# Performance work log

Measured on AMD Instinct MI355X. Metric: run time of the kernel, lower is better.

Reference implementation:

```python
import jax, jax.numpy as jnp
import numpy as np

DIM = 256
HEADS = 8
HEAD_DIM = DIM // HEADS
SCALE = HEAD_DIM ** -0.5
B, H, W = 4, 48, 48


def setup_inputs() -> dict:
    key = jax.random.key(0)
    ks = jax.random.split(key, 10)
    s = 1.0 / np.sqrt(DIM)
    return {
        "img_features": jax.random.normal(ks[0], (B, DIM, H, W), jnp.float32),
        "radar_features": jax.random.normal(ks[1], (B, DIM, H, W), jnp.float32),
        "uncertainty_mask": jax.random.uniform(ks[2], (B, 1, H, W), jnp.float32),
        "Wq_img": jax.random.normal(ks[3], (DIM, DIM), jnp.float32) * s,
        "Wkv_radar": jax.random.normal(ks[4], (DIM, 2 * DIM), jnp.float32) * s,
        "Wq_radar": jax.random.normal(ks[5], (DIM, DIM), jnp.float32) * s,
        "Wkv_img": jax.random.normal(ks[6], (DIM, 2 * DIM), jnp.float32) * s,
        "Wp_img": jax.random.normal(ks[7], (DIM, DIM), jnp.float32) * s,
        "bp_img": jnp.zeros((DIM,), jnp.float32),
        "Wp_radar": jax.random.normal(ks[8], (DIM, DIM), jnp.float32) * s,
        "bp_radar": jnp.zeros((DIM,), jnp.float32),
    }


def _heads(x, b, n):
    # (B, N, C) -> (B, heads, N, head_dim)
    return x.reshape(b, n, HEADS, HEAD_DIM).transpose(0, 2, 1, 3)


def _cross_attn(q_seq, kv_seq, Wq, Wkv, uw=None):
    b, n, c = q_seq.shape
    q = _heads(q_seq @ Wq, b, n)                      # (B,h,N,d)
    kv = (kv_seq @ Wkv).reshape(b, n, 2, HEADS, HEAD_DIM)
    k = kv[:, :, 0].transpose(0, 2, 1, 3)             # (B,h,N,d)
    v = kv[:, :, 1].transpose(0, 2, 1, 3)
    scores = jnp.einsum("bhnd,bhmd->bhnm", q, k) * SCALE
    if uw is not None:
        scores = scores * uw                          # (B,1,N,1) broadcast
    p = jax.nn.softmax(scores, axis=-1)
    out = jnp.einsum("bhnm,bhmd->bhnd", p, v)
    return out.transpose(0, 2, 1, 3).reshape(b, n, c)


def reference(img_features, radar_features, uncertainty_mask,
              Wq_img, Wkv_radar, Wq_radar, Wkv_img,
              Wp_img, bp_img, Wp_radar, bp_radar):
    b, c, h, w = img_features.shape
    n = h * w
    img_seq = img_features.reshape(b, c, n).transpose(0, 2, 1)    # (B,N,C)
    radar_seq = radar_features.reshape(b, c, n).transpose(0, 2, 1)

    # uncertainty weight: (B,1,N,1), scales query rows before softmax
    u_seq = uncertainty_mask.reshape(b, 1, n).transpose(0, 2, 1)  # (B,N,1)
    uw = (1.0 / (u_seq + 1e-6))[:, None, :, :]

    img_att = _cross_attn(img_seq, radar_seq, Wq_img, Wkv_radar, uw)
    img_att = img_att @ Wp_img + bp_img

    radar_att = _cross_attn(radar_seq, img_seq, Wq_radar, Wkv_img, None)
    radar_att = radar_att @ Wp_radar + bp_radar

    img_out = img_att.transpose(0, 2, 1).reshape(b, c, h, w)
    radar_out = radar_att.transpose(0, 2, 1).reshape(b, c, h, w)
    return img_out, radar_out
```

## Files before the change

kernel.cpp:

```cpp
#include <hip/hip_runtime.h>
#include <math.h>

#define NB    4
#define CDIM  256
#define NSEQ  2304
#define NHEAD 8
#define HD    32
#define QSCALE (0.17677669529663687f * 1.4426950408889634f)
#define INV2048 4.8828125e-4f
#define FIXMAX 12.0f

typedef _Float16 f16;
typedef _Float16 f16x8 __attribute__((ext_vector_type(8)));
typedef _Float16 f16x4 __attribute__((ext_vector_type(4)));
typedef _Float16 f16x2 __attribute__((ext_vector_type(2)));
typedef float    f32x4 __attribute__((ext_vector_type(4)));
typedef float    f32x16 __attribute__((ext_vector_type(16)));
typedef unsigned u32x4 __attribute__((ext_vector_type(4)));

__device__ __forceinline__ float fast_exp2(float x) {
#if __has_builtin(__builtin_amdgcn_exp2f)
  return __builtin_amdgcn_exp2f(x);
#else
  return exp2f(x);
#endif
}

__device__ __forceinline__ unsigned pkrtz(float a, float b) {
#if __has_builtin(__builtin_amdgcn_cvt_pkrtz)
  auto h = __builtin_amdgcn_cvt_pkrtz(a, b);
  return __builtin_bit_cast(unsigned, h);
#else
  f16x2 h; h[0] = (f16)a; h[1] = (f16)b;
  return __builtin_bit_cast(unsigned, h);
#endif
}

__device__ __forceinline__ void plswap(unsigned &a, unsigned &b) {
#if __has_builtin(__builtin_amdgcn_permlane32_swap)
  auto r = __builtin_amdgcn_permlane32_swap(a, b, false, false);
  a = r[0]; b = r[1];
#else
  asm("v_permlane32_swap_b32 %0, %1" : "+v"(a), "+v"(b));
#endif
}

__device__ __forceinline__ float cross_fmax(float v) {
  unsigned a = __builtin_bit_cast(unsigned, v), b;
  asm("v_mov_b32 %0, %1" : "=v"(b) : "v"(a));
  plswap(a, b);
  return fmaxf(__builtin_bit_cast(float, a), __builtin_bit_cast(float, b));
}
__device__ __forceinline__ float cross_add(float v) {
  unsigned a = __builtin_bit_cast(unsigned, v), b;
  asm("v_mov_b32 %0, %1" : "=v"(b) : "v"(a));
  plswap(a, b);
  return __builtin_bit_cast(float, a) + __builtin_bit_cast(float, b);
}

__global__ __launch_bounds__(256) void prep_split(
    const float* __restrict__ X0, const float* __restrict__ X1,
    const float* __restrict__ Wq0, const float* __restrict__ Wkv0,
    const float* __restrict__ Wp0, const float* __restrict__ Wq1,
    const float* __restrict__ Wkv1, const float* __restrict__ Wp1,
    f16* __restrict__ X16h, f16* __restrict__ X16l,
    f16* __restrict__ WTh, f16* __restrict__ WTl)
{
  __shared__ float Ls[64][65];
  const int t = threadIdx.x;
  const int id = blockIdx.x;

  const float* in; int incols, c0, col0; size_t obase; f16 *oh, *ol;
  float scale = 1.f;
  if (id < 1152) {
    int mb = id / 144, rem = id % 144;
    int ct = rem / 36, nt = rem % 36;
    int mod = mb >> 2, b = mb & 3;
    in = (mod ? X1 : X0) + (size_t)b * 256 * NSEQ;
    incols = NSEQ; c0 = ct * 64; col0 = nt * 64;
    obase = (size_t)mb * NSEQ + col0;
    oh = X16h; ol = X16l;
  } else {
    int wid = id - 1152;
    int mod = wid >> 6, r = wid & 63;
    int jt, ct2, rowoff;
    if (r < 16) {
      in = mod ? Wq1 : Wq0; incols = 256; jt = r >> 2; ct2 = r & 3;
      rowoff = 0; scale = QSCALE;
    } else if (r < 48) {
      int rr = r - 16;
      in = mod ? Wkv1 : Wkv0; incols = 512; jt = rr >> 2; ct2 = rr & 3;
      rowoff = 256;
    } else {
      int rr = r - 48;
      in = mod ? Wp1 : Wp0; incols = 256; jt = rr >> 2; ct2 = rr & 3;
      rowoff = 768;
    }
    c0 = ct2 * 64; col0 = jt * 64;
    obase = (size_t)mod * 1024 + rowoff + col0;
    oh = WTh; ol = WTl;
  }

#pragma unroll
  for (int i = 0; i < 4; ++i) {
    int cl = (t >> 4) + i * 16;
    int n4 = (t & 15) * 4;
    *(float4*)&Ls[cl][n4] =
        *(const float4*)(in + (size_t)(c0 + cl) * incols + col0 + n4);
  }
  __syncthreads();
#pragma unroll
  for (int i = 0; i < 4; ++i) {
    int ll = (t >> 4) + i * 16;
    int c4 = (t & 15) * 4;
    f16x4 hv, lv;
#pragma unroll
    for (int j = 0; j < 4; ++j) {
      float v = Ls[c4 + j][ll] * scale;
      f16 hh = (f16)v;
      hv[j] = hh;
      lv[j] = (f16)((v - (float)hh) * 2048.0f);
    }
    size_t o = (obase + ll) * 256 + c0 + c4;
    *(f16x4*)(oh + o) = hv;
    *(f16x4*)(ol + o) = lv;
  }
}

__global__ __launch_bounds__(256) void proj_qkv_mfma(
    const f16* __restrict__ X16h, const f16* __restrict__ X16l,
    const f16* __restrict__ WTh, const f16* __restrict__ WTl,
    f16* __restrict__ Qh, f16* __restrict__ Ql,
    f16* __restrict__ Kh, f16* __restrict__ Kl, f16* __restrict__ Vt)
{
  __shared__ f16 WhS[128][32];
  __shared__ f16 WlS[128][32];
  __shared__ f16 XhS[64][32];
  __shared__ f16 XlS[64][32];

  const int zz = blockIdx.z, mod = zz >> 2, b = zz & 3;
  const int n0 = blockIdx.y * 64, j0 = blockIdx.x * 128;
  const int t = threadIdx.x;
  const int wave = t >> 6, lane = t & 63;
  const int col = lane & 15, quad = lane >> 4;

  const bool need_lo = (j0 < 256) ? (mod == 0)
                     : (j0 < 512) ? (mod == 1) : false;

  const size_t wbase = (size_t)mod * 1024 + j0;
  const size_t xbase = ((size_t)(mod * NB + b) * NSEQ + n0) * 256;

  f32x4 am[2][4], ac[2][4];
#pragma unroll
  for (int s = 0; s < 2; ++s)
#pragma unroll
    for (int tt = 0; tt < 4; ++tt) {
      am[s][tt] = (f32x4){0.f, 0.f, 0.f, 0.f};
      ac[s][tt] = (f32x4){0.f, 0.f, 0.f, 0.f};
    }

  const int wrow = t >> 1, wseg = (t & 1) * 16;
  const int xrow = t >> 2, xseg = (t & 3) * 8;

  for (int c0 = 0; c0 < 256; c0 += 32) {
    __syncthreads();
    *(f16x8*)&WhS[wrow][wseg] =
        *(const f16x8*)(WTh + (wbase + wrow) * 256 + c0 + wseg);
    *(f16x8*)&WhS[wrow][wseg + 8] =
        *(const f16x8*)(WTh + (wbase + wrow) * 256 + c0 + wseg + 8);
    *(f16x8*)&XhS[xrow][xseg] =
        *(const f16x8*)(X16h + xbase + (size_t)xrow * 256 + c0 + xseg);
    if (need_lo) {
      *(f16x8*)&WlS[wrow][wseg] =
          *(const f16x8*)(WTl + (wbase + wrow) * 256 + c0 + wseg);
      *(f16x8*)&WlS[wrow][wseg + 8] =
          *(const f16x8*)(WTl + (wbase + wrow) * 256 + c0 + wseg + 8);
      *(f16x8*)&XlS[xrow][xseg] =
          *(const f16x8*)(X16l + xbase + (size_t)xrow * 256 + c0 + xseg);
    }
    __syncthreads();

    f16x8 Ah0 = *(const f16x8*)&WhS[wave * 32 + col][quad * 8];
    f16x8 Ah1 = *(const f16x8*)&WhS[wave * 32 + 16 + col][quad * 8];
    if (need_lo) {
      f16x8 Al0 = *(const f16x8*)&WlS[wave * 32 + col][quad * 8];
      f16x8 Al1 = *(const f16x8*)&WlS[wave * 32 + 16 + col][quad * 8];
#pragma unroll
      for (int tt = 0; tt < 4; ++tt) {
        f16x8 Bh = *(const f16x8*)&XhS[tt * 16 + col][quad * 8];
        f16x8 Bl = *(const f16x8*)&XlS[tt * 16 + col][quad * 8];
        am[0][tt] = __builtin_amdgcn_mfma_f32_16x16x32_f16(Ah0, Bh, am[0][tt], 0, 0, 0);
        ac[0][tt] = __builtin_amdgcn_mfma_f32_16x16x32_f16(Ah0, Bl, ac[0][tt], 0, 0, 0);
        ac[0][tt] = __builtin_amdgcn_mfma_f32_16x16x32_f16(Al0, Bh, ac[0][tt], 0, 0, 0);
        am[1][tt] = __builtin_amdgcn_mfma_f32_16x16x32_f16(Ah1, Bh, am[1][tt], 0, 0, 0);
        ac[1][tt] = __builtin_amdgcn_mfma_f32_16x16x32_f16(Ah1, Bl, ac[1][tt], 0, 0, 0);
        ac[1][tt] = __builtin_amdgcn_mfma_f32_16x16x32_f16(Al1, Bh, ac[1][tt], 0, 0, 0);
      }
    } else {
#pragma unroll
      for (int tt = 0; tt < 4; ++tt) {
        f16x8 Bh = *(const f16x8*)&XhS[tt * 16 + col][quad * 8];
        am[0][tt] = __builtin_amdgcn_mfma_f32_16x16x32_f16(Ah0, Bh, am[0][tt], 0, 0, 0);
        am[1][tt] = __builtin_amdgcn_mfma_f32_16x16x32_f16(Ah1, Bh, am[1][tt], 0, 0, 0);
      }
    }
  }

#pragma unroll
  for (int s = 0; s < 2; ++s) {
    const int jq = j0 + wave * 32 + s * 16 + quad * 4;
#pragma unroll
    for (int tt = 0; tt < 4; ++tt) {
      const int n = n0 + tt * 16 + col;
      float v[4];
#pragma unroll
      for (int r = 0; r < 4; ++r)
        v[r] = need_lo ? fmaf(ac[s][tt][r], INV2048, am[s][tt][r])
                       : am[s][tt][r];
      if (jq < 256) {
        f16x4 hv, lv;
#pragma unroll
        for (int r = 0; r < 4; ++r) {
          f16 hh = (f16)v[r]; hv[r] = hh;
          lv[r] = (f16)((v[r] - (float)hh) * 2048.0f);
        }
        *(f16x4*)(Qh + ((size_t)(mod * NB + b) * NSEQ + n) * 256 + jq) = hv;
        if (mod == 0)
          *(f16x4*)(Ql + ((size_t)b * NSEQ + n) * 256 + jq) = lv;
      } else if (jq < 512) {
        f16x4 hv, lv;
#pragma unroll
        for (int r = 0; r < 4; ++r) {
          f16 hh = (f16)v[r]; hv[r] = hh;
          lv[r] = (f16)((v[r] - (float)hh) * 2048.0f);
        }
        *(f16x4*)(Kh + ((size_t)(mod * NB + b) * NSEQ + n) * 256 + (jq - 256)) = hv;
        if (mod == 1)
          *(f16x4*)(Kl + ((size_t)b * NSEQ + n) * 256 + (jq - 256)) = lv;
      } else {
#pragma unroll
        for (int r = 0; r < 4; ++r)
          Vt[((size_t)(mod * NB + b) * 256 + (jq - 512 + r)) * NSEQ + n] = (f16)v[r];
      }
    }
  }
}

__global__ __launch_bounds__(256, 4) void attn_mfma(
    const f16* __restrict__ Qh, const f16* __restrict__ Ql,
    const f16* __restrict__ Kh, const f16* __restrict__ Kl,
    const f16* __restrict__ Vt, const float* __restrict__ U,
    f16* __restrict__ A16)
{
  __shared__ __align__(16) f16 KhS[2][64][40];
  __shared__ __align__(16) f16 KlS[2][64][40];
  __shared__ __align__(16) f16 VtS[2][32][72];

  const int branch = blockIdx.x;
  const int bh = blockIdx.y, b = bh >> 3, h = bh & 7;
  const int tid = threadIdx.x;
  const int wave = tid >> 6, lane = tid & 63;
  const int c32 = lane & 31, hi = lane >> 5;
  const int qr = blockIdx.z * 128 + wave * 32 + c32;

  unsigned da = (lane < 32) ? 1u : 2u;
  unsigned db = (lane < 32) ? 3u : 4u;
  plswap(da, db);
  const bool varA = (__builtin_amdgcn_readfirstlane((int)da) == 1);

  const int qmod = branch, kmod = 1 - branch;
  const size_t qbase = (size_t)(qmod * NB + b) * NSEQ * 256;
  const size_t kbase = (size_t)(kmod * NB + b) * NSEQ;
  const size_t kbaseL = (size_t)b * NSEQ;
  const size_t vbase = (size_t)(kmod * NB + b) * 256;

  f16x8 bqh[2], bql[2] = {};
  bqh[0] = *(const f16x8*)(Qh + qbase + (size_t)qr * 256 + h * HD + hi * 8);
  bqh[1] = *(const f16x8*)(Qh + qbase + (size_t)qr * 256 + h * HD + 16 + hi * 8);
  float uw = 1.0f;
  if (branch == 0) {
    const size_t qbaseL = (size_t)b * NSEQ * 256;
    bql[0] = *(const f16x8*)(Ql + qbaseL + (size_t)qr * 256 + h * HD + hi * 8);
    bql[1] = *(const f16x8*)(Ql + qbaseL + (size_t)qr * 256 + h * HD + 16 + hi * 8);
    uw = 1.0f / (U[b * NSEQ + qr] + 1e-6f);
  }

  float m = -1e30f, l = 0.f;
  f32x16 oc;
#pragma unroll
  for (int r = 0; r < 16; ++r) oc[r] = 0.f;
  f32x16 z16;
#pragma unroll
  for (int r = 0; r < 16; ++r) z16[r] = 0.f;

  const int krow = tid >> 2, kseg = (tid & 3) * 8;
  const int vrow = tid >> 3, vseg = (tid & 7) * 8;

  const f16* gKh = Kh + (kbase + krow) * 256 + h * HD + kseg;
  const f16* gKl = Kl + (kbaseL + krow) * 256 + h * HD + kseg;
  const f16* gV  = Vt + (vbase + h * HD + vrow) * NSEQ + vseg;

  f16x8 pkh = *(const f16x8*)gKh;
  f16x8 pkl = {};
  if (branch == 0) pkl = *(const f16x8*)gKl;
  f16x8 pv = *(const f16x8*)gV;

  for (int c = 0; c < NSEQ / 64; ++c) {
    const int cur = c & 1;
    *(f16x8*)&KhS[cur][krow][kseg] = pkh;
    if (branch == 0) *(f16x8*)&KlS[cur][krow][kseg] = pkl;
    *(f16x8*)&VtS[cur][vrow][vseg] = pv;
    const int kn = (c + 1 < NSEQ / 64) ? (c + 1) * 64 : 0;
    pkh = *(const f16x8*)(gKh + (size_t)kn * 256);
    if (branch == 0) pkl = *(const f16x8*)(gKl + (size_t)kn * 256);
    pv = *(const f16x8*)(gV + kn);
    __syncthreads();

    float p[2][16];
    __builtin_amdgcn_s_setprio(1);
#pragma unroll
    for (int kt = 0; kt < 2; ++kt) {
      f32x16 acc;
      if (branch == 0) {
        f16x8 ah0 = *(const f16x8*)&KhS[cur][kt * 32 + c32][hi * 8];
        f16x8 ah1 = *(const f16x8*)&KhS[cur][kt * 32 + c32][16 + hi * 8];
        f16x8 al0 = *(const f16x8*)&KlS[cur][kt * 32 + c32][hi * 8];
        f16x8 al1 = *(const f16x8*)&KlS[cur][kt * 32 + c32][16 + hi * 8];
        acc = __builtin_amdgcn_mfma_f32_32x32x16_f16(ah0, bql[0], z16, 0, 0, 0);
        acc = __builtin_amdgcn_mfma_f32_32x32x16_f16(al0, bqh[0], acc, 0, 0, 0);
        acc = __builtin_amdgcn_mfma_f32_32x32x16_f16(ah1, bql[1], acc, 0, 0, 0);
        acc = __builtin_amdgcn_mfma_f32_32x32x16_f16(al1, bqh[1], acc, 0, 0, 0);
#pragma unroll
        for (int r = 0; r < 16; ++r) acc[r] *= INV2048;
        acc = __builtin_amdgcn_mfma_f32_32x32x16_f16(ah0, bqh[0], acc, 0, 0, 0);
        acc = __builtin_amdgcn_mfma_f32_32x32x16_f16(ah1, bqh[1], acc, 0, 0, 0);
      } else {
        f16x8 ah0 = *(const f16x8*)&KhS[cur][kt * 32 + c32][hi * 8];
        f16x8 ah1 = *(const f16x8*)&KhS[cur][kt * 32 + c32][16 + hi * 8];
        acc = __builtin_amdgcn_mfma_f32_32x32x16_f16(ah0, bqh[0], z16, 0, 0, 0);
        acc = __builtin_amdgcn_mfma_f32_32x32x16_f16(ah1, bqh[1], acc, 0, 0, 0);
      }
#pragma unroll
      for (int r = 0; r < 16; ++r) p[kt][r] = acc[r];
    }
    __builtin_amdgcn_s_setprio(0);

    if (branch == 0) {
      float t8[8];
#pragma unroll
      for (int i = 0; i < 8; ++i)
        t8[i] = fmaxf(fmaxf(fmaxf(p[0][i], p[0][i + 8]), p[1][i]), p[1][i + 8]);
#pragma unroll
      for (int s = 4; s > 0; s >>= 1)
#pragma unroll
        for (int i = 0; i < s; ++i) t8[i] = fmaxf(t8[i], t8[i + s]);
      float cmax = cross_fmax(t8[0] * uw);
      const bool nore = __all(cmax <= m);
      const float mn = nore ? m : fmaxf(m, cmax);
      float sA = 0.f, sB = 0.f;
#pragma unroll
      for (int kt = 0; kt < 2; ++kt)
#pragma unroll
        for (int r = 0; r < 16; r += 2) {
          float eA = fast_exp2(fmaf(p[kt][r],     uw, -mn));
          float eB = fast_exp2(fmaf(p[kt][r + 1], uw, -mn));
          p[kt][r] = eA; p[kt][r + 1] = eB;
          sA += eA; sB += eB;
        }
      float ls = cross_add(sA + sB);
      if (nore) {
        l += ls;
      } else {
        const float alpha = fast_exp2(m - mn);
        m = mn;
        l = fmaf(l, alpha, ls);
#pragma unroll
        for (int r = 0; r < 16; ++r) oc[r] *= alpha;
      }
    } else {
      float sA = 0.f, sB = 0.f;
#pragma unroll
      for (int kt = 0; kt < 2; ++kt)
#pragma unroll
        for (int r = 0; r < 16; r += 2) {
          float eA = fast_exp2(p[kt][r]     - FIXMAX);
          float eB = fast_exp2(p[kt][r + 1] - FIXMAX);
          p[kt][r] = eA; p[kt][r + 1] = eB;
          sA += eA; sB += eB;
        }
      l += cross_add(sA + sB);
    }

    unsigned pk[2][4][2];
#pragma unroll
    for (int kt = 0; kt < 2; ++kt)
#pragma unroll
      for (int Q = 0; Q < 4; ++Q) {
        pk[kt][Q][0] = pkrtz(p[kt][4 * Q],     p[kt][4 * Q + 1]);
        pk[kt][Q][1] = pkrtz(p[kt][4 * Q + 2], p[kt][4 * Q + 3]);
      }

    __builtin_amdgcn_s_setprio(1);
#pragma unroll
    for (int km = 0; km < 4; ++km) {
      const int kt = km >> 1, Qb = (km & 1) * 2;
      unsigned w0 = pk[kt][Qb][0],     w1 = pk[kt][Qb][1];
      unsigned w2 = pk[kt][Qb + 1][0], w3 = pk[kt][Qb + 1][1];
      if (varA) { plswap(w0, w2); plswap(w1, w3); }
      else      { plswap(w2, w0); plswap(w3, w1); }
      u32x4 uv = {w0, w1, w2, w3};
      f16x8 bp = __builtin_bit_cast(f16x8, uv);
      f16x8 av = *(const f16x8*)&VtS[cur][c32][km * 16 + hi * 8];
      oc = __builtin_amdgcn_mfma_f32_32x32x16_f16(av, bp, oc, 0, 0, 0);
    }
    __builtin_amdgcn_s_setprio(0);
  }

  const float iv = 1.0f / l;
  f16* d0 = A16 + (((size_t)(branch * NB + b) * NSEQ) + qr) * 256 + h * HD + hi * 4;
#pragma unroll
  for (int g = 0; g < 4; ++g) {
    f16x4 o;
#pragma unroll
    for (int r = 0; r < 4; ++r) o[r] = (f16)(oc[4 * g + r] * iv);
    *(f16x4*)(d0 + 8 * g) = o;
  }
}

__global__ __launch_bounds__(256) void proj_out_mfma(
    const f16* __restrict__ A16, const f16* __restrict__ WTh,
    const f16* __restrict__ WTl, const float* __restrict__ bp0,
    const float* __restrict__ bp1, float* __restrict__ O)
{
  __shared__ f16 WhS[128][32];
  __shared__ f16 WlS[128][32];
  __shared__ f16 AS[64][32];

  const int zz = blockIdx.z, mod = zz >> 2, b = zz & 3;
  const int n0 = blockIdx.y * 64, j0 = blockIdx.x * 128;
  const int t = threadIdx.x;
  const int wave = t >> 6, lane = t & 63;
  const int col = lane & 15, quad = lane >> 4;

  const size_t wbase = (size_t)mod * 1024 + 768 + j0;
  const size_t abase = ((size_t)(mod * NB + b) * NSEQ + n0) * 256;

  f32x4 am[2][4], ac[2][4];
#pragma unroll
  for (int s = 0; s < 2; ++s)
#pragma unroll
    for (int tt = 0; tt < 4; ++tt) {
      am[s][tt] = (f32x4){0.f, 0.f, 0.f, 0.f};
      ac[s][tt] = (f32x4){0.f, 0.f, 0.f, 0.f};
    }

  const int wrow = t >> 1, wseg = (t & 1) * 16;
  const int xrow = t >> 2, xseg = (t & 3) * 8;

  for (int c0 = 0; c0 < 256; c0 += 32) {
    __syncthreads();
    *(f16x8*)&WhS[wrow][wseg] =
        *(const f16x8*)(WTh + (wbase + wrow) * 256 + c0 + wseg);
    *(f16x8*)&WhS[wrow][wseg + 8] =
        *(const f16x8*)(WTh + (wbase + wrow) * 256 + c0 + wseg + 8);
    *(f16x8*)&WlS[wrow][wseg] =
        *(const f16x8*)(WTl + (wbase + wrow) * 256 + c0 + wseg);
    *(f16x8*)&WlS[wrow][wseg + 8] =
        *(const f16x8*)(WTl + (wbase + wrow) * 256 + c0 + wseg + 8);
    *(f16x8*)&AS[xrow][xseg] =
        *(const f16x8*)(A16 + abase + (size_t)xrow * 256 + c0 + xseg);
    __syncthreads();

    f16x8 Ah0 = *(const f16x8*)&WhS[wave * 32 + col][quad * 8];
    f16x8 Al0 = *(const f16x8*)&WlS[wave * 32 + col][quad * 8];
    f16x8 Ah1 = *(const f16x8*)&WhS[wave * 32 + 16 + col][quad * 8];
    f16x8 Al1 = *(const f16x8*)&WlS[wave * 32 + 16 + col][quad * 8];
#pragma unroll
    for (int tt = 0; tt < 4; ++tt) {
      f16x8 Bh = *(const f16x8*)&AS[tt * 16 + col][quad * 8];
      am[0][tt] = __builtin_amdgcn_mfma_f32_16x16x32_f16(Ah0, Bh, am[0][tt], 0, 0, 0);
      ac[0][tt] = __builtin_amdgcn_mfma_f32_16x16x32_f16(Al0, Bh, ac[0][tt], 0, 0, 0);
      am[1][tt] = __builtin_amdgcn_mfma_f32_16x16x32_f16(Ah1, Bh, am[1][tt], 0, 0, 0);
      ac[1][tt] = __builtin_amdgcn_mfma_f32_16x16x32_f16(Al1, Bh, ac[1][tt], 0, 0, 0);
    }
  }

  const float* bp = mod ? bp1 : bp0;
  float* Ob = O + (size_t)(mod * NB + b) * CDIM * NSEQ;
#pragma unroll
  for (int s = 0; s < 2; ++s) {
    const int jq = j0 + wave * 32 + s * 16 + quad * 4;
    const float4 bias = *(const float4*)(bp + jq);
    const float bias_r[4] = {bias.x, bias.y, bias.z, bias.w};
#pragma unroll
    for (int tt = 0; tt < 4; ++tt) {
      const int n = n0 + tt * 16 + col;
#pragma unroll
      for (int r = 0; r < 4; ++r) {
        float v = fmaf(ac[s][tt][r], INV2048, am[s][tt][r]) + bias_r[r];
        Ob[(size_t)(jq + r) * NSEQ + n] = v;
      }
    }
  }
}

extern "C" void kernel_launch(void* const* d_in, const int* in_sizes, int n_in,
                              void* d_out, int out_size, void* d_ws, size_t ws_size,
                              hipStream_t stream) {
  (void)in_sizes; (void)n_in; (void)out_size; (void)ws_size;
  const float* img     = (const float*)d_in[0];
  const float* rad     = (const float*)d_in[1];
  const float* U       = (const float*)d_in[2];
  const float* Wq_img  = (const float*)d_in[3];
  const float* Wkv_rad = (const float*)d_in[4];
  const float* Wq_rad  = (const float*)d_in[5];
  const float* Wkv_img = (const float*)d_in[6];
  const float* Wp_img  = (const float*)d_in[7];
  const float* bp_img  = (const float*)d_in[8];
  const float* Wp_rad  = (const float*)d_in[9];
  const float* bp_rad  = (const float*)d_in[10];
  float* out = (float*)d_out;

  const size_t NE = (size_t)2 * NB * NSEQ * 256;
  const size_t WE = (size_t)2 * 1024 * 256;
  f16* X16h = (f16*)d_ws;
  f16* X16l = X16h + NE;
  f16* WTh  = X16l + NE;
  f16* WTl  = WTh + WE;
  f16* Qh   = WTl + WE;
  f16* Ql   = Qh + NE;
  f16* Kh   = Ql + NE / 2;
  f16* Kl   = Kh + NE;
  f16* Vt   = Kl + NE / 2;
  f16* A16  = Vt + NE;

  prep_split<<<dim3(1280), 256, 0, stream>>>(
      img, rad, Wq_img, Wkv_img, Wp_img, Wq_rad, Wkv_rad, Wp_rad,
      X16h, X16l, WTh, WTl);

  dim3 gp(6, 36, 2 * NB);
  proj_qkv_mfma<<<gp, 256, 0, stream>>>(X16h, X16l, WTh, WTl,
                                        Qh, Ql, Kh, Kl, Vt);

  dim3 ga(2, NB * NHEAD, NSEQ / 128);
  attn_mfma<<<ga, 256, 0, stream>>>(Qh, Ql, Kh, Kl, Vt, U, A16);

  dim3 go(2, 36, 2 * NB);
  proj_out_mfma<<<go, 256, 0, stream>>>(A16, WTh, WTl, bp_img, bp_rad, out);
}
```

Measured before the change: 276.9 us.

## Load K/V fragments directly from global memory, dropping LDS staging and barriers

After: 429.5 us. 55.1% more time.

```diff
diff --git a/kernel.cpp b/kernel.cpp
--- a/kernel.cpp
+++ b/kernel.cpp
@@ -222,7 +222,7 @@
 #pragma unroll
         for (int r = 0; r < 4; ++r) {
           f16 hh = (f16)v[r]; hv[r] = hh;
-          lv[r] = (f16)((v[r] - (float)hh) * 2048.0f);
+          lv[r] = (f16)(v[r] - (float)hh);
         }
         *(f16x4*)(Qh + ((size_t)(mod * NB + b) * NSEQ + n) * 256 + jq) = hv;
         if (mod == 0)
@@ -232,7 +232,7 @@
 #pragma unroll
         for (int r = 0; r < 4; ++r) {
           f16 hh = (f16)v[r]; hv[r] = hh;
-          lv[r] = (f16)((v[r] - (float)hh) * 2048.0f);
+          lv[r] = (f16)(v[r] - (float)hh);
         }
         *(f16x4*)(Kh + ((size_t)(mod * NB + b) * NSEQ + n) * 256 + (jq - 256)) = hv;
         if (mod == 1)
@@ -252,10 +252,6 @@
     const f16* __restrict__ Vt, const float* __restrict__ U,
     f16* __restrict__ A16)
 {
-  __shared__ __align__(16) f16 KhS[2][64][40];
-  __shared__ __align__(16) f16 KlS[2][64][40];
-  __shared__ __align__(16) f16 VtS[2][32][72];
-
   const int branch = blockIdx.x;
   const int bh = blockIdx.y, b = bh >> 3, h = bh & 7;
   const int tid = threadIdx.x;
@@ -271,7 +267,6 @@
   const int qmod = branch, kmod = 1 - branch;
   const size_t qbase = (size_t)(qmod * NB + b) * NSEQ * 256;
   const size_t kbase = (size_t)(kmod * NB + b) * NSEQ;
-  const size_t kbaseL = (size_t)b * NSEQ;
   const size_t vbase = (size_t)(kmod * NB + b) * 256;
 
   f16x8 bqh[2], bql[2] = {};
@@ -293,57 +288,50 @@
 #pragma unroll
   for (int r = 0; r < 16; ++r) z16[r] = 0.f;
 
-  const int krow = tid >> 2, kseg = (tid & 3) * 8;
-  const int vrow = tid >> 3, vseg = (tid & 7) * 8;
-
-  const f16* gKh = Kh + (kbase + krow) * 256 + h * HD + kseg;
-  const f16* gKl = Kl + (kbaseL + krow) * 256 + h * HD + kseg;
-  const f16* gV  = Vt + (vbase + h * HD + vrow) * NSEQ + vseg;
-
-  f16x8 pkh = *(const f16x8*)gKh;
-  f16x8 pkl = {};
-  if (branch == 0) pkl = *(const f16x8*)gKl;
-  f16x8 pv = *(const f16x8*)gV;
-
-  for (int c = 0; c < NSEQ / 64; ++c) {
-    const int cur = c & 1;
-    *(f16x8*)&KhS[cur][krow][kseg] = pkh;
-    if (branch == 0) *(f16x8*)&KlS[cur][krow][kseg] = pkl;
-    *(f16x8*)&VtS[cur][vrow][vseg] = pv;
-    const int kn = (c + 1 < NSEQ / 64) ? (c + 1) * 64 : 0;
-    pkh = *(const f16x8*)(gKh + (size_t)kn * 256);
-    if (branch == 0) pkl = *(const f16x8*)(gKl + (size_t)kn * 256);
-    pv = *(const f16x8*)(gV + kn);
-    __syncthreads();
+  const f16* kp  = Kh + (kbase + c32) * 256 + h * HD + hi * 8;
+  const f16* klp = Kl + ((size_t)b * NSEQ + c32) * 256 + h * HD + hi * 8;
+  const f16* vp  = Vt + (vbase + h * HD + c32) * NSEQ + hi * 8;
+
+  for (int k0 = 0; k0 < NSEQ; k0 += 64) {
+    f16x8 ah0[2], ah1[2], al0[2], al1[2];
+#pragma unroll
+    for (int kt = 0; kt < 2; ++kt) {
+      const f16* kr = kp + (size_t)(kt * 32) * 256;
+      ah0[kt] = *(const f16x8*)kr;
+      ah1[kt] = *(const f16x8*)(kr + 16);
+    }
+    if (branch == 0) {
+#pragma unroll
+      for (int kt = 0; kt < 2; ++kt) {
+        const f16* kr = klp + (size_t)(kt * 32) * 256;
+        al0[kt] = *(const f16x8*)kr;
+        al1[kt] = *(const f16x8*)(kr + 16);
+      }
+    }
+    f16x8 av[4];
+#pragma unroll
+    for (int km = 0; km < 4; ++km)
+      av[km] = *(const f16x8*)(vp + km * 16);
+    kp += 64 * 256; klp += 64 * 256; vp += 64;
 
     float p[2][16];
-    __builtin_amdgcn_s_setprio(1);
 #pragma unroll
     for (int kt = 0; kt < 2; ++kt) {
       f32x16 acc;
       if (branch == 0) {
-        f16x8 ah0 = *(const f16x8*)&KhS[cur][kt * 32 + c32][hi * 8];
-        f16x8 ah1 = *(const f16x8*)&KhS[cur][kt * 32 + c32][16 + hi * 8];
-        f16x8 al0 = *(const f16x8*)&KlS[cur][kt * 32 + c32][hi * 8];
-        f16x8 al1 = *(const f16x8*)&KlS[cur][kt * 32 + c32][16 + hi * 8];
-        acc = __builtin_amdgcn_mfma_f32_32x32x16_f16(ah0, bql[0], z16, 0, 0, 0);
-        acc = __builtin_amdgcn_mfma_f32_32x32x16_f16(al0, bqh[0], acc, 0, 0, 0);
-        acc = __builtin_amdgcn_mfma_f32_32x32x16_f16(ah1, bql[1], acc, 0, 0, 0);
-        acc = __builtin_amdgcn_mfma_f32_32x32x16_f16(al1, bqh[1], acc, 0, 0, 0);
-#pragma unroll
-        for (int r = 0; r < 16; ++r) acc[r] *= INV2048;
-        acc = __builtin_amdgcn_mfma_f32_32x32x16_f16(ah0, bqh[0], acc, 0, 0, 0);
-        acc = __builtin_amdgcn_mfma_f32_32x32x16_f16(ah1, bqh[1], acc, 0, 0, 0);
+        acc = __builtin_amdgcn_mfma_f32_32x32x16_f16(ah0[kt], bql[0], z16, 0, 0, 0);
+        acc = __builtin_amdgcn_mfma_f32_32x32x16_f16(al0[kt], bqh[0], acc, 0, 0, 0);
+        acc = __builtin_amdgcn_mfma_f32_32x32x16_f16(ah1[kt], bql[1], acc, 0, 0, 0);
+        acc = __builtin_amdgcn_mfma_f32_32x32x16_f16(al1[kt], bqh[1], acc, 0, 0, 0);
+        acc = __builtin_amdgcn_mfma_f32_32x32x16_f16(ah0[kt], bqh[0], acc, 0, 0, 0);
+        acc = __builtin_amdgcn_mfma_f32_32x32x16_f16(ah1[kt], bqh[1], acc, 0, 0, 0);
       } else {
-        f16x8 ah0 = *(const f16x8*)&KhS[cur][kt * 32 + c32][hi * 8];
-        f16x8 ah1 = *(const f16x8*)&KhS[cur][kt * 32 + c32][16 + hi * 8];
-        acc = __builtin_amdgcn_mfma_f32_32x32x16_f16(ah0, bqh[0], z16, 0, 0, 0);
-        acc = __builtin_amdgcn_mfma_f32_32x32x16_f16(ah1, bqh[1], acc, 0, 0, 0);
+        acc = __builtin_amdgcn_mfma_f32_32x32x16_f16(ah0[kt], bqh[0], z16, 0, 0, 0);
+        acc = __builtin_amdgcn_mfma_f32_32x32x16_f16(ah1[kt], bqh[1], acc, 0, 0, 0);
       }
 #pragma unroll
       for (int r = 0; r < 16; ++r) p[kt][r] = acc[r];
     }
-    __builtin_amdgcn_s_setprio(0);
 
     if (branch == 0) {
       float t8[8];
@@ -367,13 +355,12 @@
           p[kt][r] = eA; p[kt][r + 1] = eB;
           sA += eA; sB += eB;
         }
-      float ls = cross_add(sA + sB);
       if (nore) {
-        l += ls;
+        l += sA + sB;
       } else {
         const float alpha = fast_exp2(m - mn);
         m = mn;
-        l = fmaf(l, alpha, ls);
+        l = fmaf(l, alpha, sA + sB);
 #pragma unroll
         for (int r = 0; r < 16; ++r) oc[r] *= alpha;
       }
@@ -388,7 +375,7 @@
           p[kt][r] = eA; p[kt][r + 1] = eB;
           sA += eA; sB += eB;
         }
-      l += cross_add(sA + sB);
+      l += sA + sB;
     }
 
     unsigned pk[2][4][2];
@@ -400,7 +387,6 @@
         pk[kt][Q][1] = pkrtz(p[kt][4 * Q + 2], p[kt][4 * Q + 3]);
       }
 
-    __builtin_amdgcn_s_setprio(1);
 #pragma unroll
     for (int km = 0; km < 4; ++km) {
       const int kt = km >> 1, Qb = (km & 1) * 2;
@@ -410,11 +396,11 @@
       else      { plswap(w2, w0); plswap(w3, w1); }
       u32x4 uv = {w0, w1, w2, w3};
       f16x8 bp = __builtin_bit_cast(f16x8, uv);
-      f16x8 av = *(const f16x8*)&VtS[cur][c32][km * 16 + hi * 8];
-      oc = __builtin_amdgcn_mfma_f32_32x32x16_f16(av, bp, oc, 0, 0, 0);
-    }
-    __builtin_amdgcn_s_setprio(0);
-  }
+      oc = __builtin_amdgcn_mfma_f32_32x32x16_f16(av[km], bp, oc, 0, 0, 0);
+    }
+  }
+
+  l = cross_add(l);
 
   const float iv = 1.0f / l;
   f16* d0 = A16 + (((size_t)(branch * NB + b) * NSEQ) + qr) * 256 + h * HD + hi * 4;
```
